# Kernel optimization log

Measured on AMD Instinct MI355X. Metric: run time of the kernel, lower is better.

The kernel has to match this reference:

```python
import jax, jax.numpy as jnp
import numpy as np

N_NODES = 100000
N_EDGES = 3200000
N_GRAPHS = 512
EPS = 1e-5

def _glorot(key, shape):
    fan_in, fan_out = shape[0], shape[1]
    lim = (6.0 / (fan_in + fan_out)) ** 0.5
    return jax.random.uniform(key, shape, jnp.float32, -lim, lim)

def setup_inputs() -> dict:
    key = jax.random.key(0)
    ks = jax.random.split(key, 16)
    x = jax.random.normal(ks[0], (N_NODES, 6), jnp.float32)
    edge_index = jax.random.randint(ks[1], (2, N_EDGES), 0, N_NODES, jnp.int32)
    batch = jnp.sort(jax.random.randint(ks[2], (N_NODES,), 0, N_GRAPHS, jnp.int32))
    params = {
        'Wl1': _glorot(ks[3], (6, 64)),  'bl1': jnp.zeros((64,)), 'Wr1': _glorot(ks[4], (6, 64)),
        'Wl2': _glorot(ks[5], (64, 64)), 'bl2': jnp.zeros((64,)), 'Wr2': _glorot(ks[6], (64, 64)),
        'Wl3': _glorot(ks[7], (64, 64)), 'bl3': jnp.zeros((64,)), 'Wr3': _glorot(ks[8], (64, 64)),
        'g1': jnp.ones((64,)), 'be1': jnp.zeros((64,)),
        'g2': jnp.ones((64,)), 'be2': jnp.zeros((64,)),
        'g3': jnp.ones((64,)), 'be3': jnp.zeros((64,)),
        'W_lin1': _glorot(ks[9], (128, 64)), 'b_lin1': jnp.zeros((64,)),
        'W_lin2': _glorot(ks[10], (64, 2)),  'b_lin2': jnp.zeros((2,)),
    }
    return {'x': x, 'edge_index': edge_index, 'batch': batch, **params}

def _sage(x, src, dst, Wl, bl, Wr):
    # PyG SAGEConv (mean aggr): lin_l(mean_{j in N(i)} x_j) + lin_r(x_i)
    msg_sum = jax.ops.segment_sum(x[src], dst, num_segments=N_NODES)
    cnt = jax.ops.segment_sum(jnp.ones((src.shape[0],), x.dtype), dst, num_segments=N_NODES)
    mean = msg_sum / jnp.maximum(cnt, 1.0)[:, None]
    return mean @ Wl + bl + x @ Wr

def _bn(x, g, b):
    # training-mode BatchNorm over nodes
    mu = jnp.mean(x, axis=0)
    var = jnp.var(x, axis=0)
    return (x - mu) * jax.lax.rsqrt(var + EPS) * g + b

def reference(x, edge_index, batch, Wl1, bl1, Wr1, Wl2, bl2, Wr2, Wl3, bl3, Wr3,
              g1, be1, g2, be2, g3, be3, W_lin1, b_lin1, W_lin2, b_lin2):
    src, dst = edge_index[0], edge_index[1]
    h = jax.nn.relu(_bn(_sage(x, src, dst, Wl1, bl1, Wr1), g1, be1))
    h = jax.nn.relu(_bn(_sage(h, src, dst, Wl2, bl2, Wr2), g2, be2))
    h = jax.nn.relu(_bn(_sage(h, src, dst, Wl3, bl3, Wr3), g3, be3))
    x_max = jax.ops.segment_max(h, batch, num_segments=N_GRAPHS)
    s = jax.ops.segment_sum(h, batch, num_segments=N_GRAPHS)
    n = jax.ops.segment_sum(jnp.ones((h.shape[0],), h.dtype), batch, num_segments=N_GRAPHS)
    x_mean = s / jnp.maximum(n, 1.0)[:, None]
    z = jnp.concatenate([x_max, x_mean], axis=1)  # [G, 128]
    z = jax.nn.relu(z @ W_lin1 + b_lin1)
    # dropout is identity in eval mode
    return z @ W_lin2 + b_lin2
```

## Files before the change

kernel.cpp:

```cpp
#include <hip/hip_runtime.h>
#include <math.h>

#define NN 100000
#define NE 3200000
#define NG 512
#define NWELEM 26114
#define DRANGE 12500

__device__ __forceinline__ float b2f(unsigned short u) {
    union { float f; unsigned int i; } c; c.i = ((unsigned int)u) << 16; return c.f;
}
__device__ __forceinline__ unsigned short f2b(float f) {
    union { float f; unsigned int i; } c; c.f = f;
    unsigned int r = c.i + 0x7FFFu + ((c.i >> 16) & 1u);
    return (unsigned short)(r >> 16);
}

__global__ void k_detect_f(const unsigned short* __restrict__ u, int n,
                           int* __restrict__ c0, int* __restrict__ c1) {
    int t = blockIdx.x * blockDim.x + threadIdx.x;
    int a = 0, b = 0;
    for (int i = t; i < n; i += gridDim.x * blockDim.x) {
        float v = b2f(u[i]);
        if (!isfinite(v) || fabsf(v) > 1.0e4f) a++;
        if (((i & 1) == 0) && u[i] == 0) b++;
    }
    if (a) atomicAdd(c0, a);
    if (b) atomicAdd(c1, b);
}
__global__ void k_detect_odd(const int* __restrict__ p, int base, int n,
                             int* __restrict__ c) {
    int t = blockIdx.x * blockDim.x + threadIdx.x;
    int a = 0;
    for (int i = t; i < n; i += gridDim.x * blockDim.x)
        if (p[base + 2 * i + 1] != 0) a++;
    if (a) atomicAdd(c, a);
}
__global__ void k_flags(int* __restrict__ cnt) {
    cnt[8]  = (cnt[0] > 50 || cnt[1] > 8000) ? 1 : 0;
    cnt[9]  = (cnt[2] > 50 || cnt[3] > 1000) ? 1 : 0;
    cnt[10] = (cnt[4] < 100) ? 1 : 0;
    cnt[11] = (cnt[5] < 100) ? 1 : 0;
}

__device__ __forceinline__ int e_src(const int* ei, long e, bool i64) {
    return i64 ? ei[2 * e] : ei[e];
}
__device__ __forceinline__ int e_dst(const int* ei, long e, bool i64) {
    return i64 ? ei[2 * ((long)NE + e)] : ei[(long)NE + e];
}

__global__ void k_conv_x8(const void* __restrict__ p, float* __restrict__ dst,
                          const int* __restrict__ flags) {
    int i = blockIdx.x * blockDim.x + threadIdx.x;
    if (i >= NN * 8) return;
    int node = i >> 3, f = i & 7;
    float v = 0.f;
    if (f < 6)
        v = flags[8] ? ((const float*)p)[node * 6 + f]
                     : b2f(((const unsigned short*)p)[node * 6 + f]);
    dst[i] = v;
}
__global__ void k_conv_batch(const int* __restrict__ b, int* __restrict__ b32,
                             const int* __restrict__ flags) {
    int i = blockIdx.x * blockDim.x + threadIdx.x;
    if (i >= NN) return;
    b32[i] = flags[11] ? b[2 * i] : b[i];
}
struct WPtrs { const void* p[19]; };
__global__ void k_conv_w(WPtrs wp, float* __restrict__ dst, const int* __restrict__ flags) {
    const int L[19] = {384, 64, 384, 4096, 64, 4096, 4096, 64, 4096,
                       64, 64, 64, 64, 64, 64, 8192, 64, 128, 2};
    bool f32 = flags[9];
    int i = blockIdx.x * blockDim.x + threadIdx.x;
    if (i >= NWELEM) return;
    int ti = 0, off = i;
    while (off >= L[ti]) { off -= L[ti]; ti++; }
    const void* p = wp.p[ti];
    dst[i] = f32 ? ((const float*)p)[off] : b2f(((const unsigned short*)p)[off]);
}

__global__ void k_hist(const int* __restrict__ ei, const int* __restrict__ flags,
                       int* __restrict__ counts) {
    long e = (long)blockIdx.x * blockDim.x + threadIdx.x;
    if (e >= NE) return;
    int d = e_dst(ei, e, flags[10]);
    if ((unsigned)d < NN) atomicAdd(&counts[d], 1);
}
__global__ void k_scat8(const int* __restrict__ ei, const int* __restrict__ flags,
                        int* __restrict__ cursor, int* __restrict__ csr) {
    int xcd = blockIdx.x & 7;
    int grp = blockIdx.x >> 3;
    int ngrp = gridDim.x >> 3;
    int lo = xcd * DRANGE, hi = lo + DRANGE;
    bool i64 = flags[10];
    for (long e = (long)grp * blockDim.x + threadIdx.x; e < NE;
         e += (long)ngrp * blockDim.x) {
        int d = e_dst(ei, e, i64);
        if (d >= lo && d < hi) {
            int s = e_src(ei, e, i64);
            int p = atomicAdd(&cursor[d], 1);
            if (p >= 0 && p < NE) csr[p] = ((unsigned)s < NN) ? s : 0;
        }
    }
}

__global__ void k_scan_block(const int* __restrict__ counts, int* __restrict__ inblk,
                             int* __restrict__ btot) {
    __shared__ int s[256];
    int t = threadIdx.x;
    int idx = blockIdx.x * 256 + t;
    int v = (idx < NN) ? counts[idx] : 0;
    s[t] = v;
    __syncthreads();
    for (int off = 1; off < 256; off <<= 1) {
        int x = (t >= off) ? s[t - off] : 0;
        __syncthreads();
        s[t] += x;
        __syncthreads();
    }
    if (idx < NN) inblk[idx] = s[t] - v;
    if (t == 255) btot[blockIdx.x] = s[255];
}
__global__ void k_scan_top(const int* __restrict__ btot, int* __restrict__ boff, int nb) {
    __shared__ int s[512];
    int t = threadIdx.x;
    int v = (t < nb) ? btot[t] : 0;
    s[t] = v;
    __syncthreads();
    for (int off = 1; off < 512; off <<= 1) {
        int x = (t >= off) ? s[t - off] : 0;
        __syncthreads();
        s[t] += x;
        __syncthreads();
    }
    if (t < nb) boff[t] = s[t] - v;
}
__global__ void k_scan_final(const int* __restrict__ inblk, const int* __restrict__ boff,
                             int* __restrict__ rowptr, int* __restrict__ cursor) {
    int idx = blockIdx.x * 256 + threadIdx.x;
    if (idx < NN) {
        int r = inblk[idx] + boff[blockIdx.x];
        rowptr[idx] = r;
        cursor[idx] = r;
    }
    if (idx == 0) rowptr[NN] = NE;
}

__global__ void k_agg6(const float* __restrict__ x8, const int* __restrict__ rowptr,
                       const int* __restrict__ csr, float* __restrict__ agg) {
    int gt = blockIdx.x * blockDim.x + threadIdx.x;
    int node = gt >> 6;
    if (node >= NN) return;
    int lane = threadIdx.x & 63;
    int f = lane & 7, es = lane >> 3;
    int r0 = rowptr[node], r1 = rowptr[node + 1];
    float acc = 0.f;
    for (int e = r0 + es; e < r1; e += 8) {
        int s = csr[e];
        acc += x8[s * 8 + f];
    }
    acc += __shfl_xor(acc, 8);
    acc += __shfl_xor(acc, 16);
    acc += __shfl_xor(acc, 32);
    int deg = r1 - r0;
    if (lane < 8) agg[node * 8 + lane] = acc / (float)(deg > 0 ? deg : 1);
}
__global__ void k_agg64b(const unsigned short* __restrict__ hb,
                         const int* __restrict__ rowptr,
                         const int* __restrict__ csr, float* __restrict__ agg) {
    int gt = blockIdx.x * blockDim.x + threadIdx.x;
    int node = gt >> 6;
    if (node >= NN) return;
    int lane = threadIdx.x & 63;
    int r0 = rowptr[node], r1 = rowptr[node + 1];
    float acc = 0.f;
    int e = r0;
    for (; e + 3 < r1; e += 4) {
        int s0 = csr[e], s1 = csr[e + 1], s2 = csr[e + 2], s3 = csr[e + 3];
        acc += b2f(hb[(long)s0 * 64 + lane]);
        acc += b2f(hb[(long)s1 * 64 + lane]);
        acc += b2f(hb[(long)s2 * 64 + lane]);
        acc += b2f(hb[(long)s3 * 64 + lane]);
    }
    for (; e < r1; e++) acc += b2f(hb[(long)csr[e] * 64 + lane]);
    int deg = r1 - r0;
    agg[(long)node * 64 + lane] = acc / (float)(deg > 0 ? deg : 1);
}

__global__ void k_mm1(const float* __restrict__ agg6, const float* __restrict__ x8,
                      const float* __restrict__ Wl, const float* __restrict__ bl,
                      const float* __restrict__ Wr, float* __restrict__ pre,
                      double* __restrict__ part) {
    __shared__ float wl[6 * 64], wr[6 * 64];
    int t = threadIdx.x;
    for (int j = t; j < 384; j += 256) { wl[j] = Wl[j]; wr[j] = Wr[j]; }
    __syncthreads();
    int o = t & 63, rs = t >> 6;
    float bo = bl[o];
    double sm = 0.0, sq = 0.0;
    for (int i0 = blockIdx.x * 4; i0 < NN; i0 += gridDim.x * 4) {
        int i = i0 + rs;
        if (i < NN) {
            const float* m = &agg6[i * 8];
            const float* xr = &x8[i * 8];
            float p = bo;
#pragma unroll
            for (int k = 0; k < 6; k++) p += m[k] * wl[k * 64 + o] + xr[k] * wr[k * 64 + o];
            pre[(long)i * 64 + o] = p;
            sm += p;
            sq += (double)p * p;
        }
    }
    __shared__ double sd[256];
    sd[t] = sm; __syncthreads();
    if (t < 128) sd[t] += sd[t + 128];
    __syncthreads();
    if (t < 64) part[blockIdx.x * 128 + t] = sd[t] + sd[t + 64];
    __syncthreads();
    sd[t] = sq; __syncthreads();
    if (t < 128) sd[t] += sd[t + 128];
    __syncthreads();
    if (t < 64) part[blockIdx.x * 128 + 64 + t] = sd[t] + sd[t + 64];
}

__global__ void k_mm64b(const float* __restrict__ agg, const unsigned short* __restrict__ hb,
                        const float* __restrict__ Wl, const float* __restrict__ bl,
                        const float* __restrict__ Wr, float* __restrict__ pre,
                        double* __restrict__ part) {
    __shared__ float wl[4096], wr[4096];
    int t = threadIdx.x;
    for (int j = t; j < 4096; j += 256) { wl[j] = Wl[j]; wr[j] = Wr[j]; }
    __syncthreads();
    int o = t & 63, wv = t >> 6;
    float bo = bl[o];
    double sm = 0.0, sq = 0.0;
    for (int i0 = blockIdx.x * 16; i0 < NN; i0 += gridDim.x * 16) {
        long i = i0 + wv * 4;
        const float* m0 = agg + i * 64;
        const unsigned short* h0 = hb + i * 64;
        float a0 = bo, a1 = bo, a2 = bo, a3 = bo;
#pragma unroll 8
        for (int k = 0; k < 64; k++) {
            float wlv = wl[k * 64 + o];
            float wrv = wr[k * 64 + o];
            a0 += m0[k]       * wlv + b2f(h0[k])       * wrv;
            a1 += m0[64 + k]  * wlv + b2f(h0[64 + k])  * wrv;
            a2 += m0[128 + k] * wlv + b2f(h0[128 + k]) * wrv;
            a3 += m0[192 + k] * wlv + b2f(h0[192 + k]) * wrv;
        }
        pre[(i + 0) * 64 + o] = a0;
        pre[(i + 1) * 64 + o] = a1;
        pre[(i + 2) * 64 + o] = a2;
        pre[(i + 3) * 64 + o] = a3;
        sm += (double)a0 + (double)a1 + (double)a2 + (double)a3;
        sq += (double)a0 * a0 + (double)a1 * a1 + (double)a2 * a2 + (double)a3 * a3;
    }
    __shared__ double sd[256];
    sd[t] = sm; __syncthreads();
    if (t < 128) sd[t] += sd[t + 128];
    __syncthreads();
    if (t < 64) part[blockIdx.x * 128 + t] = sd[t] + sd[t + 64];
    __syncthreads();
    sd[t] = sq; __syncthreads();
    if (t < 128) sd[t] += sd[t + 128];
    __syncthreads();
    if (t < 64) part[blockIdx.x * 128 + 64 + t] = sd[t] + sd[t + 64];
}

__global__ void k_statred_p(const double* __restrict__ part, int nb,
                            float* __restrict__ mu, float* __restrict__ inv) {
    int c = blockIdx.x;
    int t = threadIdx.x;
    double sm = 0.0, sq = 0.0;
    for (int b = t; b < nb; b += 256) {
        sm += part[(long)b * 128 + c];
        sq += part[(long)b * 128 + 64 + c];
    }
    __shared__ double s1[256], s2[256];
    s1[t] = sm; s2[t] = sq;
    __syncthreads();
    for (int off = 128; off > 0; off >>= 1) {
        if (t < off) { s1[t] += s1[t + off]; s2[t] += s2[t + off]; }
        __syncthreads();
    }
    if (t == 0) {
        double m = s1[0] / (double)NN;
        double v = s2[0] / (double)NN - m * m;
        mu[c] = (float)m;
        inv[c] = (float)rsqrt(v + 1e-5);
    }
}

__global__ void k_bnrelu(float4* __restrict__ pre, ushort4* __restrict__ hb,
                         const float* __restrict__ mu, const float* __restrict__ inv,
                         const float* __restrict__ g, const float* __restrict__ be) {
    long idx = (long)blockIdx.x * blockDim.x + threadIdx.x;
    if (idx >= (long)NN * 16) return;
    int c = ((int)idx & 15) * 4;
    float4 p = pre[idx];
    p.x = fmaxf((p.x - mu[c + 0]) * inv[c + 0] * g[c + 0] + be[c + 0], 0.f);
    p.y = fmaxf((p.y - mu[c + 1]) * inv[c + 1] * g[c + 1] + be[c + 1], 0.f);
    p.z = fmaxf((p.z - mu[c + 2]) * inv[c + 2] * g[c + 2] + be[c + 2], 0.f);
    p.w = fmaxf((p.w - mu[c + 3]) * inv[c + 3] * g[c + 3] + be[c + 3], 0.f);
    pre[idx] = p;
    ushort4 u;
    u.x = f2b(p.x); u.y = f2b(p.y); u.z = f2b(p.z); u.w = f2b(p.w);
    hb[idx] = u;
}

__device__ __forceinline__ int lowb(const int* b, int n, int key) {
    int lo = 0, hi = n;
    while (lo < hi) {
        int m = (lo + hi) >> 1;
        if (b[m] < key) lo = m + 1; else hi = m;
    }
    return lo;
}
__global__ void k_pool(const float* __restrict__ h, const int* __restrict__ batch,
                       float* __restrict__ z) {
    int g = blockIdx.x;
    int t = threadIdx.x;
    int lo = lowb(batch, NN, g);
    int hi = lowb(batch, NN, g + 1);
    int c = t & 63, rs = t >> 6;
    float mx = 0.f, sm = 0.f;
    for (int i = lo + rs; i < hi; i += 4) {
        float v = h[(long)i * 64 + c];
        mx = fmaxf(mx, v);
        sm += v;
    }
    __shared__ float s1[256], s2[256];
    s1[t] = mx; s2[t] = sm;
    __syncthreads();
    if (t < 128) { s1[t] = fmaxf(s1[t], s1[t + 128]); s2[t] += s2[t + 128]; }
    __syncthreads();
    if (t < 64) {
        float M = fmaxf(s1[t], s1[t + 64]);
        float S = s2[t] + s2[t + 64];
        int n = hi - lo;
        z[g * 128 + t] = M;
        z[g * 128 + 64 + t] = S / (float)(n > 0 ? n : 1);
    }
}
__global__ void k_mlp(const float* __restrict__ z, const float* __restrict__ W1,
                      const float* __restrict__ b1, const float* __restrict__ W2,
                      const float* __restrict__ b2, float* __restrict__ out) {
    int g = blockIdx.x, t = threadIdx.x;
    __shared__ float zr[128], hid[64];
    zr[t] = z[g * 128 + t];
    zr[t + 64] = z[g * 128 + 64 + t];
    __syncthreads();
    float a = b1[t];
#pragma unroll 8
    for (int k = 0; k < 128; k++) a += zr[k] * W1[k * 64 + t];
    hid[t] = fmaxf(a, 0.f);
    __syncthreads();
    if (t < 2) {
        float o = b2[t];
#pragma unroll
        for (int k = 0; k < 64; k++) o += hid[k] * W2[k * 2 + t];
        out[g * 2 + t] = o;
    }
}

static inline char* alignup(char* p, size_t a) {
    return (char*)(((uintptr_t)p + a - 1) & ~(uintptr_t)(a - 1));
}

extern "C" void kernel_launch(void* const* d_in, const int* in_sizes, int n_in,
                              void* d_out, int out_size, void* d_ws, size_t ws_size,
                              hipStream_t stream) {
    float* out = (float*)d_out;

    char* w = (char*)d_ws;
    int* dcnt   = (int*)w;            w = alignup(w + 64, 256);
    int* counts = (int*)w;            w = alignup(w + NN * 4, 256);
    int* cursor = (int*)w;            w = alignup(w + NN * 4, 256);
    int* inblk  = (int*)w;            w = alignup(w + NN * 4, 256);
    int* btot   = (int*)w;            w = alignup(w + 512 * 4, 256);
    int* boff   = (int*)w;            w = alignup(w + 512 * 4, 256);
    int* rowptr = (int*)w;            w = alignup(w + (NN + 1) * 4, 256);
    int* csr    = (int*)w;            w = alignup(w + (size_t)NE * 4, 256);
    float* agg  = (float*)w;          w = alignup(w + (size_t)NN * 64 * 4, 256);
    float* hcur = (float*)w;          w = alignup(w + (size_t)NN * 64 * 4, 256);
    unsigned short* hb = (unsigned short*)w; w = alignup(w + (size_t)NN * 64 * 2, 256);
    double* part = (double*)w;        w = alignup(w + 1024 * 128 * 8, 256);
    float* mu   = (float*)w;          w = alignup(w + 64 * 4, 256);
    float* inv  = (float*)w;          w = alignup(w + 64 * 4, 256);
    float* z    = (float*)w;          w = alignup(w + NG * 128 * 4, 256);
    float* wb   = (float*)w;          w = alignup(w + NWELEM * 4, 256);
    int* batch32 = (int*)w;           w = alignup(w + NN * 4, 256);

    float* x8 = agg + 3200000;

    const int* ei  = (const int*)d_in[1];
    const int* bat = (const int*)d_in[2];
    WPtrs wp;
    for (int i = 0; i < 19; i++) wp.p[i] = d_in[3 + i];

    const float* Wl1 = wb + 0,     *bl1 = wb + 384,   *Wr1 = wb + 448;
    const float* Wl2 = wb + 832,   *bl2 = wb + 4928,  *Wr2 = wb + 4992;
    const float* Wl3 = wb + 9088,  *bl3 = wb + 13184, *Wr3 = wb + 13248;
    const float* g1  = wb + 17344, *be1 = wb + 17408;
    const float* g2  = wb + 17472, *be2 = wb + 17536;
    const float* g3  = wb + 17600, *be3 = wb + 17664;
    const float* W_lin1 = wb + 17728, *b_lin1 = wb + 25920;
    const float* W_lin2 = wb + 25984, *b_lin2 = wb + 26112;

    const int NB_SCAN = (NN + 255) / 256;
    const int MMG1 = 1024;
    const int MMG  = 1024;
    const int BNB = ((NN * 16) + 255) / 256;
    const int AGG_GRID = (NN * 64 + 255) / 256;

    hipMemsetAsync(dcnt, 0, 64, stream);
    hipMemsetAsync(counts, 0, NN * 4, stream);

    k_detect_f<<<64, 256, 0, stream>>>((const unsigned short*)d_in[0], 65536, dcnt + 0, dcnt + 1);
    k_detect_f<<<16, 256, 0, stream>>>((const unsigned short*)d_in[6], 4096, dcnt + 2, dcnt + 3);
    k_detect_odd<<<16, 256, 0, stream>>>(ei, 1000, 8192, dcnt + 4);
    k_detect_odd<<<16, 256, 0, stream>>>(bat, 40000, 8192, dcnt + 5);
    k_flags<<<1, 1, 0, stream>>>(dcnt);

    k_conv_x8<<<(NN * 8 + 255) / 256, 256, 0, stream>>>(d_in[0], x8, dcnt);
    k_conv_batch<<<(NN + 255) / 256, 256, 0, stream>>>(bat, batch32, dcnt);
    k_conv_w<<<(NWELEM + 255) / 256, 256, 0, stream>>>(wp, wb, dcnt);

    k_hist<<<(NE + 255) / 256, 256, 0, stream>>>(ei, dcnt, counts);
    k_scan_block<<<NB_SCAN, 256, 0, stream>>>(counts, inblk, btot);
    k_scan_top<<<1, 512, 0, stream>>>(btot, boff, NB_SCAN);
    k_scan_final<<<NB_SCAN, 256, 0, stream>>>(inblk, boff, rowptr, cursor);
    k_scat8<<<1024, 256, 0, stream>>>(ei, dcnt, cursor, csr);

    k_agg6<<<AGG_GRID, 256, 0, stream>>>(x8, rowptr, csr, agg);
    k_mm1<<<MMG1, 256, 0, stream>>>(agg, x8, Wl1, bl1, Wr1, hcur, part);
    k_statred_p<<<64, 256, 0, stream>>>(part, MMG1, mu, inv);
    k_bnrelu<<<BNB, 256, 0, stream>>>((float4*)hcur, (ushort4*)hb, mu, inv, g1, be1);

    k_agg64b<<<AGG_GRID, 256, 0, stream>>>(hb, rowptr, csr, agg);
    k_mm64b<<<MMG, 256, 0, stream>>>(agg, hb, Wl2, bl2, Wr2, hcur, part);
    k_statred_p<<<64, 256, 0, stream>>>(part, MMG, mu, inv);
    k_bnrelu<<<BNB, 256, 0, stream>>>((float4*)hcur, (ushort4*)hb, mu, inv, g2, be2);

    k_agg64b<<<AGG_GRID, 256, 0, stream>>>(hb, rowptr, csr, agg);
    k_mm64b<<<MMG, 256, 0, stream>>>(agg, hb, Wl3, bl3, Wr3, hcur, part);
    k_statred_p<<<64, 256, 0, stream>>>(part, MMG, mu, inv);
    k_bnrelu<<<BNB, 256, 0, stream>>>((float4*)hcur, (ushort4*)hb, mu, inv, g3, be3);

    k_pool<<<NG, 256, 0, stream>>>(hcur, batch32, z);
    k_mlp<<<NG, 64, 0, stream>>>(z, W_lin1, b_lin1, W_lin2, b_lin2, out);
}
```

Measured before the change: 848.0 us.

## Two-pass bucketed CSR build and half-wave bf16x2 neighbour gather

Replaces the XCD-filtered scatter, in which every block scanned all edges, with a two-pass binning scheme. Edges are first grouped into 49 coarse destination buckets of 2048 nodes each, written as packed (dst,src) pairs into a reused buffer. A second pass then scatters them into the CSR with per-node atomics over contiguous bucket ranges, cutting redundant edge reads and giving the atomics better locality. The 64-feature aggregation now has each half-wave process alternate edges, loading two bf16 values per lane and combining the halves with a shuffle. The cost is an extra 25.6MB intermediate write and read, plus partial lane idling on odd degrees.

```diff
diff --git a/kernel.cpp b/kernel.cpp
--- a/kernel.cpp
+++ b/kernel.cpp
@@ -5,7 +5,7 @@
 #define NE 3200000
 #define NG 512
 #define NWELEM 26114
-#define DRANGE 12500
+#define NBUK 49
 
 __device__ __forceinline__ float b2f(unsigned short u) {
     union { float f; unsigned int i; } c; c.i = ((unsigned int)u) << 16; return c.f;
@@ -87,23 +87,6 @@
     int d = e_dst(ei, e, flags[10]);
     if ((unsigned)d < NN) atomicAdd(&counts[d], 1);
 }
-__global__ void k_scat8(const int* __restrict__ ei, const int* __restrict__ flags,
-                        int* __restrict__ cursor, int* __restrict__ csr) {
-    int xcd = blockIdx.x & 7;
-    int grp = blockIdx.x >> 3;
-    int ngrp = gridDim.x >> 3;
-    int lo = xcd * DRANGE, hi = lo + DRANGE;
-    bool i64 = flags[10];
-    for (long e = (long)grp * blockDim.x + threadIdx.x; e < NE;
-         e += (long)ngrp * blockDim.x) {
-        int d = e_dst(ei, e, i64);
-        if (d >= lo && d < hi) {
-            int s = e_src(ei, e, i64);
-            int p = atomicAdd(&cursor[d], 1);
-            if (p >= 0 && p < NE) csr[p] = ((unsigned)s < NN) ? s : 0;
-        }
-    }
-}
 
 __global__ void k_scan_block(const int* __restrict__ counts, int* __restrict__ inblk,
                              int* __restrict__ btot) {
@@ -145,6 +128,59 @@
         cursor[idx] = r;
     }
     if (idx == 0) rowptr[NN] = NE;
+}
+__global__ void k_bukinit(const int* __restrict__ rowptr, int* __restrict__ bukcur) {
+    int t = threadIdx.x;
+    if (t < NBUK) bukcur[t] = rowptr[t * 2048];
+}
+
+__global__ void k_binA(const int* __restrict__ ei, const int* __restrict__ flags,
+                       int* __restrict__ bukcur, unsigned long long* __restrict__ binbuf) {
+    __shared__ int lh[NBUK], lbase[NBUK], lcur[NBUK];
+    int t = threadIdx.x;
+    bool i64 = flags[10];
+    const long chunk = (NE + gridDim.x - 1) / gridDim.x;
+    long e0 = (long)blockIdx.x * chunk;
+    long e1 = e0 + chunk; if (e1 > NE) e1 = NE;
+    for (int b = t; b < NBUK; b += 256) lh[b] = 0;
+    __syncthreads();
+    for (long e = e0 + t; e < e1; e += 256) {
+        int d = e_dst(ei, e, i64);
+        if ((unsigned)d < NN) atomicAdd(&lh[d >> 11], 1);
+    }
+    __syncthreads();
+    for (int b = t; b < NBUK; b += 256) {
+        lbase[b] = lh[b] ? atomicAdd(&bukcur[b], lh[b]) : 0;
+        lcur[b] = 0;
+    }
+    __syncthreads();
+    for (long e = e0 + t; e < e1; e += 256) {
+        int d = e_dst(ei, e, i64);
+        if ((unsigned)d < NN) {
+            int s = e_src(ei, e, i64);
+            int b = d >> 11;
+            int off = atomicAdd(&lcur[b], 1);
+            unsigned long long v = ((unsigned long long)(unsigned)d << 32) |
+                                   (unsigned)(((unsigned)s < NN) ? s : 0);
+            __builtin_nontemporal_store(v, &binbuf[(long)lbase[b] + off]);
+        }
+    }
+}
+
+__global__ void k_binB(const unsigned long long* __restrict__ binbuf,
+                       int* __restrict__ cursor, int* __restrict__ csr) {
+    int x = blockIdx.x & 7;
+    int g = blockIdx.x >> 3;
+    int ng = gridDim.x >> 3;
+    long lo = (long)x * (NE / 8), hi = lo + (NE / 8);
+    for (long e = lo + (long)g * blockDim.x + threadIdx.x; e < hi;
+         e += (long)ng * blockDim.x) {
+        unsigned long long v = __builtin_nontemporal_load(&binbuf[e]);
+        int d = (int)(v >> 32);
+        int s = (int)(v & 0xffffffffu);
+        int p = atomicAdd(&cursor[d], 1);
+        if (p >= 0 && p < NE) csr[p] = s;
+    }
 }
 
 __global__ void k_agg6(const float* __restrict__ x8, const int* __restrict__ rowptr,
@@ -173,19 +209,27 @@
     int node = gt >> 6;
     if (node >= NN) return;
     int lane = threadIdx.x & 63;
+    int c2 = lane & 31;
+    int half = lane >> 5;
     int r0 = rowptr[node], r1 = rowptr[node + 1];
-    float acc = 0.f;
-    int e = r0;
-    for (; e + 3 < r1; e += 4) {
-        int s0 = csr[e], s1 = csr[e + 1], s2 = csr[e + 2], s3 = csr[e + 3];
-        acc += b2f(hb[(long)s0 * 64 + lane]);
-        acc += b2f(hb[(long)s1 * 64 + lane]);
-        acc += b2f(hb[(long)s2 * 64 + lane]);
-        acc += b2f(hb[(long)s3 * 64 + lane]);
-    }
-    for (; e < r1; e++) acc += b2f(hb[(long)csr[e] * 64 + lane]);
-    int deg = r1 - r0;
-    agg[(long)node * 64 + lane] = acc / (float)(deg > 0 ? deg : 1);
+    float ax = 0.f, ay = 0.f;
+    for (int e = r0; e < r1; e += 2) {
+        int er = e + half;
+        if (er < r1) {
+            int s = csr[er];
+            unsigned u = *(const unsigned*)&hb[(long)s * 64 + 2 * c2];
+            ax += b2f((unsigned short)(u & 0xffffu));
+            ay += b2f((unsigned short)(u >> 16));
+        }
+    }
+    ax += __shfl_xor(ax, 32);
+    ay += __shfl_xor(ay, 32);
+    if (half == 0) {
+        int deg = r1 - r0;
+        float inv = 1.0f / (float)(deg > 0 ? deg : 1);
+        float2 o; o.x = ax * inv; o.y = ay * inv;
+        *(float2*)&agg[(long)node * 64 + 2 * c2] = o;
+    }
 }
 
 __global__ void k_mm1(const float* __restrict__ agg6, const float* __restrict__ x8,
@@ -375,6 +419,7 @@
 
     char* w = (char*)d_ws;
     int* dcnt   = (int*)w;            w = alignup(w + 64, 256);
+    int* bukcur = (int*)w;            w = alignup(w + 256, 256);
     int* counts = (int*)w;            w = alignup(w + NN * 4, 256);
     int* cursor = (int*)w;            w = alignup(w + NN * 4, 256);
     int* inblk  = (int*)w;            w = alignup(w + NN * 4, 256);
@@ -393,6 +438,7 @@
     int* batch32 = (int*)w;           w = alignup(w + NN * 4, 256);
 
     float* x8 = agg + 3200000;
+    unsigned long long* binbuf = (unsigned long long*)hcur;
 
     const int* ei  = (const int*)d_in[1];
     const int* bat = (const int*)d_in[2];
@@ -431,7 +477,9 @@
     k_scan_block<<<NB_SCAN, 256, 0, stream>>>(counts, inblk, btot);
     k_scan_top<<<1, 512, 0, stream>>>(btot, boff, NB_SCAN);
     k_scan_final<<<NB_SCAN, 256, 0, stream>>>(inblk, boff, rowptr, cursor);
-    k_scat8<<<1024, 256, 0, stream>>>(ei, dcnt, cursor, csr);
+    k_bukinit<<<1, 64, 0, stream>>>(rowptr, bukcur);
+    k_binA<<<1024, 256, 0, stream>>>(ei, dcnt, bukcur, binbuf);
+    k_binB<<<1024, 256, 0, stream>>>(binbuf, cursor, csr);
 
     k_agg6<<<AGG_GRID, 256, 0, stream>>>(x8, rowptr, csr, agg);
     k_mm1<<<MMG1, 256, 0, stream>>>(agg, x8, Wl1, bl1, Wr1, hcur, part);
```

Measured after the change: 1.098 ms. +29.5%, slower.
